# Optimization experiments

Hardware: AMD Instinct MI355X
Metric: run time of the kernel (lower is better)

Reference implementation:

```python
import jax, jax.numpy as jnp
import numpy as np

M = 8192   # output rows
N = 8192   # input dim
K = 8192   # non_zero_rows (inner dim after dropping empty B rows)
NNZ_A = 256  # nonzeros per row of A (m x k)
NNZ_B = 256  # nonzeros per row of B (k x n)
BATCH = 32


def setup_inputs() -> dict:
    key = jax.random.key(0)
    k1, k2, k3, k4, k5 = jax.random.split(key, 5)
    x = jax.random.normal(k1, (N, BATCH), dtype=jnp.float32)
    a_idx = jax.random.randint(k2, (M, NNZ_A), 0, K, dtype=jnp.int32)
    a_vals = jax.random.normal(k3, (M, NNZ_A), dtype=jnp.float32) * 0.05
    b_idx = jax.random.randint(k4, (K, NNZ_B), 0, N, dtype=jnp.int32)
    b_vals = jax.random.normal(k5, (K, NNZ_B), dtype=jnp.float32) * 0.05
    return {"x": x, "a_idx": a_idx, "a_vals": a_vals, "b_idx": b_idx, "b_vals": b_vals}


def reference(x, a_idx, a_vals, b_idx, b_vals):
    # Double-sparse matvec: y = A @ (B @ x), sparse matrices in ELL form
    # (row-wise column indices + values, equivalent math to the CSR kernel).
    # B @ x: gather x rows per nonzero of B, contract over nnz axis.
    bx = jnp.einsum('kj,kjb->kb', b_vals, x[b_idx])        # [K, BATCH]
    # A @ bx: gather bx rows per nonzero of A.
    y = jnp.einsum('mj,mjb->mb', a_vals, bx[a_idx])        # [M, BATCH]
    # Match torch output layout: (1, batch, m)
    return y.T[None]
```

## Files before the change

kernel.cpp:

```cpp
#include <hip/hip_runtime.h>


#define NNZ     256
#define BATCH   32
#define ROWS    8192
#define SEGR    2048
#define NSEG    4
#define RPB     32
#define THREADS 512

typedef int      vi4 __attribute__((ext_vector_type(4)));
typedef float    vf4 __attribute__((ext_vector_type(4)));
typedef _Float16 vh2 __attribute__((ext_vector_type(2)));
typedef _Float16 vh4 __attribute__((ext_vector_type(4)));
typedef _Float16 vh8 __attribute__((ext_vector_type(8)));

union V8 { vh8 h8; vh2 h2[4]; unsigned u[4]; };

__global__ __launch_bounds__(256) void cvt_f32_f16(
    const float* __restrict__ src, _Float16* __restrict__ dst)
{
    const int i = blockIdx.x * 256 + threadIdx.x;
    const vf4 v = *(const vf4*)(src + i * 4);
    vh4 h;
    h.x = (_Float16)v.x; h.y = (_Float16)v.y;
    h.z = (_Float16)v.z; h.w = (_Float16)v.w;
    *(vh4*)(dst + i * 4) = h;
}

static __device__ __forceinline__ unsigned hpack(float f)
{
    const unsigned short u = __builtin_bit_cast(unsigned short, (_Float16)f);
    return ((unsigned)u << 16) | (unsigned)u;
}

#define PROC(K, BB)                                                           \
    do {                                                                      \
        const int k_ = (K);                                                   \
        V8 xv_;                                                               \
        xv_.h8 = *(const vh8*)(lb + ((((unsigned)k_ & 2047u) << 6) + soffb)); \
        const unsigned sel_ = ((k_ >> 11) == p) ? (BB) : 0u;                  \
        const vh2 b2_ = __builtin_bit_cast(vh2, sel_);                        \
        acc[t].h2[0] += b2_ * xv_.h2[0];                                      \
        acc[t].h2[1] += b2_ * xv_.h2[1];                                      \
        acc[t].h2[2] += b2_ * xv_.h2[2];                                      \
        acc[t].h2[3] += b2_ * xv_.h2[3];                                      \
    } while (0)

template <bool OUT16>
__global__ __launch_bounds__(THREADS, 2) void ell_spmv_lds(
    const int*      __restrict__ idx,
    const float*    __restrict__ vals,
    const _Float16* __restrict__ src,
    _Float16*       __restrict__ dst16,
    float*          __restrict__ dst32)
{
    __shared__ __attribute__((aligned(16))) _Float16 lds[SEGR * BATCH];

    const int tid   = threadIdx.x;
    const int wave  = tid >> 6;
    const int lane  = tid & 63;
    const int s     = lane & 3;
    const int q     = lane >> 2;
    const int soffb = s * 16;
    const int rbase = blockIdx.x * RPB;

    vi4      iv[4][4];
    unsigned hh[4][16];
    #pragma unroll
    for (int t = 0; t < 4; ++t) {
        const int r = rbase + wave * 4 + t;
        const vi4* i4 = (const vi4*)(idx  + (size_t)r * NNZ) + q * 4;
        const vf4* v4 = (const vf4*)(vals + (size_t)r * NNZ) + q * 4;
        vf4 vv[4];
        #pragma unroll
        for (int u = 0; u < 4; ++u) iv[t][u] = __builtin_nontemporal_load(i4 + u);
        #pragma unroll
        for (int u = 0; u < 4; ++u) vv[u]    = __builtin_nontemporal_load(v4 + u);
        #pragma unroll
        for (int u = 0; u < 4; ++u) {
            hh[t][4*u+0] = hpack(vv[u].x);
            hh[t][4*u+1] = hpack(vv[u].y);
            hh[t][4*u+2] = hpack(vv[u].z);
            hh[t][4*u+3] = hpack(vv[u].w);
        }
    }

    V8 acc[4];
    #pragma unroll
    for (int t = 0; t < 4; ++t) {
        acc[t].u[0] = 0; acc[t].u[1] = 0; acc[t].u[2] = 0; acc[t].u[3] = 0;
    }

    const char* lb = (const char*)lds;

    #pragma unroll 1
    for (int p = 0; p < NSEG; ++p) {
        __syncthreads();
        const char* gseg = (const char*)(src + (size_t)p * SEGR * BATCH);
        #pragma unroll
        for (int tch = 0; tch < 16; ++tch) {
            const int off = tch * 8192 + tid * 16;
            __builtin_amdgcn_global_load_lds(
                (const __attribute__((address_space(1))) unsigned int*)(gseg + off),
                (__attribute__((address_space(3))) unsigned int*)((char*)lds + off),
                16, 0, 0);
        }
        __syncthreads();

        #pragma unroll
        for (int t = 0; t < 4; ++t) {
            #pragma unroll
            for (int u = 0; u < 4; ++u) {
                PROC(iv[t][u].x, hh[t][4*u+0]);
                PROC(iv[t][u].y, hh[t][4*u+1]);
                PROC(iv[t][u].z, hh[t][4*u+2]);
                PROC(iv[t][u].w, hh[t][4*u+3]);
            }
        }
    }

    float* tile = (float*)lds;
    if (!OUT16) __syncthreads();

    #pragma unroll
    for (int t = 0; t < 4; ++t) {
        float a32[8];
        #pragma unroll
        for (int j = 0; j < 8; ++j) a32[j] = (float)acc[t].h8[j];
        #pragma unroll
        for (int d = 4; d < 64; d <<= 1) {
            #pragma unroll
            for (int j = 0; j < 8; ++j) a32[j] += __shfl_xor(a32[j], d);
        }
        if (OUT16) {
            if (q == 0) {
                const int r = rbase + wave * 4 + t;
                vh8 h;
                #pragma unroll
                for (int j = 0; j < 8; ++j) h[j] = (_Float16)a32[j];
                *(vh8*)(dst16 + (size_t)r * BATCH + s * 8) = h;
            }
        } else {
            if (q == 0) {
                const int rl = wave * 4 + t;
                #pragma unroll
                for (int j = 0; j < 8; ++j) tile[rl * 33 + s * 8 + j] = a32[j];
            }
        }
    }

    if (!OUT16) {
        __syncthreads();
        const int e  = tid * 2;
        const int b  = e >> 5;
        const int rr = e & 31;
        float2 v2;
        v2.x = tile[rr * 33 + b];
        v2.y = tile[(rr + 1) * 33 + b];
        *(float2*)(dst32 + (size_t)b * ROWS + rbase + rr) = v2;
    }
}

#undef PROC

extern "C" void kernel_launch(void* const* d_in, const int* in_sizes, int n_in,
                              void* d_out, int out_size, void* d_ws, size_t ws_size,
                              hipStream_t stream) {
    (void)in_sizes; (void)n_in; (void)out_size; (void)ws_size;
    const float* x      = (const float*)d_in[0];
    const int*   a_idx  = (const int*)  d_in[1];
    const float* a_vals = (const float*)d_in[2];
    const int*   b_idx  = (const int*)  d_in[3];
    const float* b_vals = (const float*)d_in[4];
    float*       out    = (float*)d_out;

    _Float16* bx16 = (_Float16*)d_ws;
    _Float16* x16  = (_Float16*)d_ws + (size_t)ROWS * BATCH;

    cvt_f32_f16<<<dim3(ROWS * BATCH / 4 / 256), dim3(256), 0, stream>>>(x, x16);
    ell_spmv_lds<true ><<<dim3(ROWS / RPB), dim3(THREADS), 0, stream>>>(
        b_idx, b_vals, x16, bx16, nullptr);
    ell_spmv_lds<false><<<dim3(ROWS / RPB), dim3(THREADS), 0, stream>>>(
        a_idx, a_vals, bx16, nullptr, out);
}
```

Measured before the change: 127.1 us.

## Fuse conversion and both SpMV passes into one persistent kernel with grid barriers

Replaces the three launches (f32-to-f16 convert, B pass, A pass) with one kernel that synchronises all 256 blocks through global atomic barriers. It also prefetches A's indices and values into registers before the second barrier so that load overlaps the barrier wait. Masked-out gathers now read a fixed LDS address instead of the real index. The aim is to remove launch gaps and tail effects between stages. The barrier only works if every block is co-resident, which holds with 256 blocks at two per CU on this part, and holding two row-register sets raises register pressure.

```diff
diff --git a/kernel.cpp b/kernel.cpp
--- a/kernel.cpp
+++ b/kernel.cpp
@@ -8,25 +8,16 @@
 #define NSEG    4
 #define RPB     32
 #define THREADS 512
+#define BLOCKS  (ROWS / RPB)
 
 typedef int      vi4 __attribute__((ext_vector_type(4)));
 typedef float    vf4 __attribute__((ext_vector_type(4)));
 typedef _Float16 vh2 __attribute__((ext_vector_type(2)));
-typedef _Float16 vh4 __attribute__((ext_vector_type(4)));
 typedef _Float16 vh8 __attribute__((ext_vector_type(8)));
 
 union V8 { vh8 h8; vh2 h2[4]; unsigned u[4]; };
 
-__global__ __launch_bounds__(256) void cvt_f32_f16(
-    const float* __restrict__ src, _Float16* __restrict__ dst)
-{
-    const int i = blockIdx.x * 256 + threadIdx.x;
-    const vf4 v = *(const vf4*)(src + i * 4);
-    vh4 h;
-    h.x = (_Float16)v.x; h.y = (_Float16)v.y;
-    h.z = (_Float16)v.z; h.w = (_Float16)v.w;
-    *(vh4*)(dst + i * 4) = h;
-}
+struct RowRegs { vi4 iv[4][4]; unsigned hh[4][16]; };
 
 static __device__ __forceinline__ unsigned hpack(float f)
 {
@@ -34,26 +25,107 @@
     return ((unsigned)u << 16) | (unsigned)u;
 }
 
-#define PROC(K, BB)                                                           \
-    do {                                                                      \
-        const int k_ = (K);                                                   \
-        V8 xv_;                                                               \
-        xv_.h8 = *(const vh8*)(lb + ((((unsigned)k_ & 2047u) << 6) + soffb)); \
-        const unsigned sel_ = ((k_ >> 11) == p) ? (BB) : 0u;                  \
-        const vh2 b2_ = __builtin_bit_cast(vh2, sel_);                        \
-        acc[t].h2[0] += b2_ * xv_.h2[0];                                      \
-        acc[t].h2[1] += b2_ * xv_.h2[1];                                      \
-        acc[t].h2[2] += b2_ * xv_.h2[2];                                      \
-        acc[t].h2[3] += b2_ * xv_.h2[3];                                      \
-    } while (0)
-
-template <bool OUT16>
-__global__ __launch_bounds__(THREADS, 2) void ell_spmv_lds(
-    const int*      __restrict__ idx,
-    const float*    __restrict__ vals,
-    const _Float16* __restrict__ src,
-    _Float16*       __restrict__ dst16,
-    float*          __restrict__ dst32)
+static __device__ __forceinline__ void load_rows(
+    const int* __restrict__ idx, const float* __restrict__ vals,
+    int r0, int q, RowRegs& R)
+{
+    #pragma unroll
+    for (int t = 0; t < 4; ++t) {
+        const vi4* i4 = (const vi4*)(idx  + (size_t)(r0 + t) * NNZ) + q * 4;
+        const vf4* v4 = (const vf4*)(vals + (size_t)(r0 + t) * NNZ) + q * 4;
+        vf4 vv[4];
+        #pragma unroll
+        for (int u = 0; u < 4; ++u) R.iv[t][u] = __builtin_nontemporal_load(i4 + u);
+        #pragma unroll
+        for (int u = 0; u < 4; ++u) vv[u]      = __builtin_nontemporal_load(v4 + u);
+        #pragma unroll
+        for (int u = 0; u < 4; ++u) {
+            R.hh[t][4*u+0] = hpack(vv[u].x);
+            R.hh[t][4*u+1] = hpack(vv[u].y);
+            R.hh[t][4*u+2] = hpack(vv[u].z);
+            R.hh[t][4*u+3] = hpack(vv[u].w);
+        }
+    }
+}
+
+static __device__ __forceinline__ void proc1(
+    int k, unsigned bb, int p, const char* lb, int soffb, V8& a)
+{
+    const bool in = (((unsigned)k >> 11) == (unsigned)p);
+    const int  ra = ((k & 2047) << 6) + soffb;
+    const int  ad = in ? ra : soffb;
+    V8 xv;
+    xv.h8 = *(const vh8*)(lb + ad);
+    const vh2 b2 = __builtin_bit_cast(vh2, in ? bb : 0u);
+    a.h2[0] += b2 * xv.h2[0];
+    a.h2[1] += b2 * xv.h2[1];
+    a.h2[2] += b2 * xv.h2[2];
+    a.h2[3] += b2 * xv.h2[3];
+}
+
+static __device__ __forceinline__ void pass4(
+    const RowRegs& R, const _Float16* __restrict__ src,
+    _Float16* lds, int tid, int soffb, V8 acc[4])
+{
+    const char* lb = (const char*)lds;
+    #pragma unroll 1
+    for (int p = 0; p < NSEG; ++p) {
+        __syncthreads();
+        const char* gseg = (const char*)(src + (size_t)p * SEGR * BATCH);
+        #pragma unroll
+        for (int tch = 0; tch < 16; ++tch) {
+            const int off = tch * 8192 + tid * 16;
+            __builtin_amdgcn_global_load_lds(
+                (const __attribute__((address_space(1))) unsigned int*)(gseg + off),
+                (__attribute__((address_space(3))) unsigned int*)((char*)lds + off),
+                16, 0, 0);
+        }
+        __syncthreads();
+
+        #pragma unroll
+        for (int t = 0; t < 4; ++t) {
+            #pragma unroll
+            for (int u = 0; u < 4; ++u) {
+                proc1(R.iv[t][u].x, R.hh[t][4*u+0], p, lb, soffb, acc[t]);
+                proc1(R.iv[t][u].y, R.hh[t][4*u+1], p, lb, soffb, acc[t]);
+                proc1(R.iv[t][u].z, R.hh[t][4*u+2], p, lb, soffb, acc[t]);
+                proc1(R.iv[t][u].w, R.hh[t][4*u+3], p, lb, soffb, acc[t]);
+            }
+        }
+    }
+}
+
+static __device__ __forceinline__ void gridbar(unsigned* bar, unsigned target)
+{
+    __syncthreads();
+    if (threadIdx.x == 0) {
+        __threadfence();
+        __hip_atomic_fetch_add(bar, 1u, __ATOMIC_ACQ_REL, __HIP_MEMORY_SCOPE_AGENT);
+        while (__hip_atomic_load(bar, __ATOMIC_ACQUIRE, __HIP_MEMORY_SCOPE_AGENT)
+               < target) {
+            __builtin_amdgcn_s_sleep(8);
+        }
+        __threadfence();
+    }
+    __syncthreads();
+}
+
+__global__ void bar_init(unsigned* bar)
+{
+    if (threadIdx.x == 0)
+        __hip_atomic_store(bar, 0u, __ATOMIC_RELEASE, __HIP_MEMORY_SCOPE_AGENT);
+}
+
+__global__ __launch_bounds__(THREADS, 2) void fused_spmv(
+    const float* __restrict__ x,
+    const int*   __restrict__ a_idx,
+    const float* __restrict__ a_vals,
+    const int*   __restrict__ b_idx,
+    const float* __restrict__ b_vals,
+    _Float16*    __restrict__ x16,
+    _Float16*    __restrict__ bx16,
+    float*       __restrict__ out,
+    unsigned*    __restrict__ bar)
 {
     __shared__ __attribute__((aligned(16))) _Float16 lds[SEGR * BATCH];
 
@@ -64,65 +136,55 @@
     const int q     = lane >> 2;
     const int soffb = s * 16;
     const int rbase = blockIdx.x * RPB;
-
-    vi4      iv[4][4];
-    unsigned hh[4][16];
-    #pragma unroll
-    for (int t = 0; t < 4; ++t) {
-        const int r = rbase + wave * 4 + t;
-        const vi4* i4 = (const vi4*)(idx  + (size_t)r * NNZ) + q * 4;
-        const vf4* v4 = (const vf4*)(vals + (size_t)r * NNZ) + q * 4;
-        vf4 vv[4];
-        #pragma unroll
-        for (int u = 0; u < 4; ++u) iv[t][u] = __builtin_nontemporal_load(i4 + u);
-        #pragma unroll
-        for (int u = 0; u < 4; ++u) vv[u]    = __builtin_nontemporal_load(v4 + u);
-        #pragma unroll
-        for (int u = 0; u < 4; ++u) {
-            hh[t][4*u+0] = hpack(vv[u].x);
-            hh[t][4*u+1] = hpack(vv[u].y);
-            hh[t][4*u+2] = hpack(vv[u].z);
-            hh[t][4*u+3] = hpack(vv[u].w);
-        }
-    }
+    const int r0    = rbase + wave * 4;
+
+    RowRegs RB;
+    load_rows(b_idx, b_vals, r0, q, RB);
+    {
+        const int gid = blockIdx.x * THREADS + tid;
+        const float2 v = ((const float2*)x)[gid];
+        vh2 h; h.x = (_Float16)v.x; h.y = (_Float16)v.y;
+        ((vh2*)x16)[gid] = h;
+    }
+    gridbar(bar, BLOCKS);
 
     V8 acc[4];
     #pragma unroll
     for (int t = 0; t < 4; ++t) {
         acc[t].u[0] = 0; acc[t].u[1] = 0; acc[t].u[2] = 0; acc[t].u[3] = 0;
     }
-
-    const char* lb = (const char*)lds;
-
-    #pragma unroll 1
-    for (int p = 0; p < NSEG; ++p) {
-        __syncthreads();
-        const char* gseg = (const char*)(src + (size_t)p * SEGR * BATCH);
-        #pragma unroll
-        for (int tch = 0; tch < 16; ++tch) {
-            const int off = tch * 8192 + tid * 16;
-            __builtin_amdgcn_global_load_lds(
-                (const __attribute__((address_space(1))) unsigned int*)(gseg + off),
-                (__attribute__((address_space(3))) unsigned int*)((char*)lds + off),
-                16, 0, 0);
-        }
-        __syncthreads();
-
-        #pragma unroll
-        for (int t = 0; t < 4; ++t) {
-            #pragma unroll
-            for (int u = 0; u < 4; ++u) {
-                PROC(iv[t][u].x, hh[t][4*u+0]);
-                PROC(iv[t][u].y, hh[t][4*u+1]);
-                PROC(iv[t][u].z, hh[t][4*u+2]);
-                PROC(iv[t][u].w, hh[t][4*u+3]);
-            }
-        }
-    }
-
+    pass4(RB, x16, lds, tid, soffb, acc);
+
+    RowRegs RA;
+    load_rows(a_idx, a_vals, r0, q, RA);
+
+    #pragma unroll
+    for (int t = 0; t < 4; ++t) {
+        float a32[8];
+        #pragma unroll
+        for (int j = 0; j < 8; ++j) a32[j] = (float)acc[t].h8[j];
+        #pragma unroll
+        for (int d = 4; d < 64; d <<= 1) {
+            #pragma unroll
+            for (int j = 0; j < 8; ++j) a32[j] += __shfl_xor(a32[j], d);
+        }
+        if (q == 0) {
+            vh8 h;
+            #pragma unroll
+            for (int j = 0; j < 8; ++j) h[j] = (_Float16)a32[j];
+            *(vh8*)(bx16 + (size_t)(r0 + t) * BATCH + s * 8) = h;
+        }
+    }
+    gridbar(bar, 2 * BLOCKS);
+
+    #pragma unroll
+    for (int t = 0; t < 4; ++t) {
+        acc[t].u[0] = 0; acc[t].u[1] = 0; acc[t].u[2] = 0; acc[t].u[3] = 0;
+    }
+    pass4(RA, bx16, lds, tid, soffb, acc);
+
+    __syncthreads();
     float* tile = (float*)lds;
-    if (!OUT16) __syncthreads();
-
     #pragma unroll
     for (int t = 0; t < 4; ++t) {
         float a32[8];
@@ -133,36 +195,23 @@
             #pragma unroll
             for (int j = 0; j < 8; ++j) a32[j] += __shfl_xor(a32[j], d);
         }
-        if (OUT16) {
-            if (q == 0) {
-                const int r = rbase + wave * 4 + t;
-                vh8 h;
-                #pragma unroll
-                for (int j = 0; j < 8; ++j) h[j] = (_Float16)a32[j];
-                *(vh8*)(dst16 + (size_t)r * BATCH + s * 8) = h;
-            }
-        } else {
-            if (q == 0) {
-                const int rl = wave * 4 + t;
-                #pragma unroll
-                for (int j = 0; j < 8; ++j) tile[rl * 33 + s * 8 + j] = a32[j];
-            }
-        }
-    }
-
-    if (!OUT16) {
-        __syncthreads();
+        if (q == 0) {
+            const int rl = wave * 4 + t;
+            #pragma unroll
+            for (int j = 0; j < 8; ++j) tile[rl * 33 + s * 8 + j] = a32[j];
+        }
+    }
+    __syncthreads();
+    {
         const int e  = tid * 2;
         const int b  = e >> 5;
         const int rr = e & 31;
         float2 v2;
         v2.x = tile[rr * 33 + b];
         v2.y = tile[(rr + 1) * 33 + b];
-        *(float2*)(dst32 + (size_t)b * ROWS + rbase + rr) = v2;
-    }
-}
-
-#undef PROC
+        *(float2*)(out + (size_t)b * ROWS + rbase + rr) = v2;
+    }
+}
 
 extern "C" void kernel_launch(void* const* d_in, const int* in_sizes, int n_in,
                               void* d_out, int out_size, void* d_ws, size_t ws_size,
@@ -176,11 +225,11 @@
     float*       out    = (float*)d_out;
 
     _Float16* bx16 = (_Float16*)d_ws;
-    _Float16* x16  = (_Float16*)d_ws + (size_t)ROWS * BATCH;
-
-    cvt_f32_f16<<<dim3(ROWS * BATCH / 4 / 256), dim3(256), 0, stream>>>(x, x16);
-    ell_spmv_lds<true ><<<dim3(ROWS / RPB), dim3(THREADS), 0, stream>>>(
-        b_idx, b_vals, x16, bx16, nullptr);
-    ell_spmv_lds<false><<<dim3(ROWS / RPB), dim3(THREADS), 0, stream>>>(
-        a_idx, a_vals, bx16, nullptr, out);
-}
+    _Float16* x16  = bx16 + (size_t)ROWS * BATCH;
+    unsigned* bar  = (unsigned*)((char*)d_ws +
+                                 (size_t)2 * ROWS * BATCH * sizeof(_Float16));
+
+    bar_init<<<dim3(1), dim3(64), 0, stream>>>(bar);
+    fused_spmv<<<dim3(BLOCKS), dim3(THREADS), 0, stream>>>(
+        x, a_idx, a_vals, b_idx, b_vals, x16, bx16, out, bar);
+}
```

Measured after the change: 184.8 us. 1.45x slower.

## Pre-bin sparse entries by segment into packed half/index words

Applied to the files above, without the earlier changes.

Adds a preprocessing kernel that converts x to fp16 and, for both A and B, reorders each row's nonzeros by which 2048-row segment of the dense operand they hit. Each entry is packed as an fp16 value plus a 16-bit index, and per-segment offsets are stored. The SpMV kernels then process only the entries for the current segment instead of masking all 256 per segment, which removes the 4x redundant gather/FMA work. The packed entries are staged in LDS, and the next segment's table load is issued early. In exchange, a pre-pass over both index arrays is added each call, LDS use rises because the entries buffer is added, and the inner loop's trip count now varies per row.

```diff
diff --git a/kernel.cpp b/kernel.cpp
--- a/kernel.cpp
+++ b/kernel.cpp
@@ -8,54 +8,108 @@
 #define NSEG    4
 #define RPB     32
 #define THREADS 512
+#define BLOCKS  (ROWS / RPB)
 
 typedef int      vi4 __attribute__((ext_vector_type(4)));
 typedef float    vf4 __attribute__((ext_vector_type(4)));
 typedef _Float16 vh2 __attribute__((ext_vector_type(2)));
-typedef _Float16 vh4 __attribute__((ext_vector_type(4)));
 typedef _Float16 vh8 __attribute__((ext_vector_type(8)));
 
 union V8 { vh8 h8; vh2 h2[4]; unsigned u[4]; };
 
-__global__ __launch_bounds__(256) void cvt_f32_f16(
-    const float* __restrict__ src, _Float16* __restrict__ dst)
+static __device__ __forceinline__ void gll16(const char* g, char* l)
 {
-    const int i = blockIdx.x * 256 + threadIdx.x;
-    const vf4 v = *(const vf4*)(src + i * 4);
-    vh4 h;
-    h.x = (_Float16)v.x; h.y = (_Float16)v.y;
-    h.z = (_Float16)v.z; h.w = (_Float16)v.w;
-    *(vh4*)(dst + i * 4) = h;
-}
-
-static __device__ __forceinline__ unsigned hpack(float f)
+    __builtin_amdgcn_global_load_lds(
+        (const __attribute__((address_space(1))) unsigned int*)g,
+        (__attribute__((address_space(3))) unsigned int*)l, 16, 0, 0);
+}
+
+__global__ __launch_bounds__(256) void bin_cvt(
+    const float* __restrict__ x,
+    const int*   __restrict__ a_idx, const float* __restrict__ a_vals,
+    const int*   __restrict__ b_idx, const float* __restrict__ b_vals,
+    _Float16* __restrict__ x16,
+    unsigned* __restrict__ bentB, unsigned long long* __restrict__ offB,
+    unsigned* __restrict__ bentA, unsigned long long* __restrict__ offA)
 {
-    const unsigned short u = __builtin_bit_cast(unsigned short, (_Float16)f);
-    return ((unsigned)u << 16) | (unsigned)u;
-}
-
-#define PROC(K, BB)                                                           \
-    do {                                                                      \
-        const int k_ = (K);                                                   \
-        V8 xv_;                                                               \
-        xv_.h8 = *(const vh8*)(lb + ((((unsigned)k_ & 2047u) << 6) + soffb)); \
-        const unsigned sel_ = ((k_ >> 11) == p) ? (BB) : 0u;                  \
-        const vh2 b2_ = __builtin_bit_cast(vh2, sel_);                        \
-        acc[t].h2[0] += b2_ * xv_.h2[0];                                      \
-        acc[t].h2[1] += b2_ * xv_.h2[1];                                      \
-        acc[t].h2[2] += b2_ * xv_.h2[2];                                      \
-        acc[t].h2[3] += b2_ * xv_.h2[3];                                      \
-    } while (0)
+    __shared__ __attribute__((aligned(16))) unsigned sent[4][NNZ];
+
+    const int tid  = threadIdx.x;
+    const int wave = tid >> 6;
+    const int lane = tid & 63;
+
+    {
+        const int gid = blockIdx.x * 256 + tid;
+        x16[gid] = (_Float16)x[gid];
+    }
+
+    const unsigned long long lt = (1ull << lane) - 1ull;
+    const int wgid = blockIdx.x * 4 + wave;
+
+    #pragma unroll
+    for (int w = 0; w < 4; ++w) {
+        const bool isB = (w < 2);
+        const int  r   = wgid + (w & 1) * 4096;
+        const int*   idx  = isB ? b_idx  : a_idx;
+        const float* vals = isB ? b_vals : a_vals;
+        unsigned*           bent = isB ? bentB : bentA;
+        unsigned long long* off  = isB ? offB  : offA;
+
+        const vi4 kk = __builtin_nontemporal_load(
+            (const vi4*)(idx + (size_t)r * NNZ) + lane);
+        const vf4 vv = __builtin_nontemporal_load(
+            (const vf4*)(vals + (size_t)r * NNZ) + lane);
+
+        unsigned c0 = 0, c1 = 0, c2 = 0, c3 = 0;
+        int sg[4]; unsigned rk[4];
+        #pragma unroll
+        for (int j = 0; j < 4; ++j) {
+            const int sgn = kk[j] >> 11;
+            const unsigned long long m0 = __ballot(sgn == 0);
+            const unsigned long long m1 = __ballot(sgn == 1);
+            const unsigned long long m2 = __ballot(sgn == 2);
+            const unsigned long long m3 = __ballot(sgn == 3);
+            rk[j] = (sgn == 0) ? c0 + (unsigned)__popcll(m0 & lt)
+                  : (sgn == 1) ? c1 + (unsigned)__popcll(m1 & lt)
+                  : (sgn == 2) ? c2 + (unsigned)__popcll(m2 & lt)
+                  :              c3 + (unsigned)__popcll(m3 & lt);
+            sg[j] = sgn;
+            c0 += (unsigned)__popcll(m0); c1 += (unsigned)__popcll(m1);
+            c2 += (unsigned)__popcll(m2); c3 += (unsigned)__popcll(m3);
+        }
+        const unsigned b1 = c0, b2 = c0 + c1, b3 = c0 + c1 + c2;
+
+        #pragma unroll
+        for (int j = 0; j < 4; ++j) {
+            const unsigned base = (sg[j] == 0) ? 0u : (sg[j] == 1) ? b1
+                                 : (sg[j] == 2) ? b2 : b3;
+            const unsigned short hv =
+                __builtin_bit_cast(unsigned short, (_Float16)vv[j]);
+            sent[wave][base + rk[j]] =
+                ((unsigned)hv << 16) | ((unsigned)kk[j] & 0xFFFFu);
+        }
+        __syncthreads();
+
+        const vi4 ob = *(const vi4*)&sent[wave][lane * 4];
+        *(vi4*)(bent + (size_t)r * NNZ + lane * 4) = ob;
+        if (lane == 0)
+            off[r] = ((unsigned long long)b1 << 16) |
+                     ((unsigned long long)b2 << 32) |
+                     ((unsigned long long)b3 << 48);
+        __syncthreads();
+    }
+}
 
 template <bool OUT16>
-__global__ __launch_bounds__(THREADS, 2) void ell_spmv_lds(
-    const int*      __restrict__ idx,
-    const float*    __restrict__ vals,
+__global__ __launch_bounds__(THREADS) void ell_spmv_bin(
+    const unsigned* __restrict__ bent,
+    const unsigned long long* __restrict__ off,
     const _Float16* __restrict__ src,
-    _Float16*       __restrict__ dst16,
-    float*          __restrict__ dst32)
+    _Float16* __restrict__ dst16,
+    float*    __restrict__ dst32)
 {
-    __shared__ __attribute__((aligned(16))) _Float16 lds[SEGR * BATCH];
+    __shared__ __attribute__((aligned(16))) _Float16 table[SEGR * BATCH];
+    __shared__ __attribute__((aligned(16))) unsigned entl[RPB * NNZ];
 
     const int tid   = threadIdx.x;
     const int wave  = tid >> 6;
@@ -64,64 +118,67 @@
     const int q     = lane >> 2;
     const int soffb = s * 16;
     const int rbase = blockIdx.x * RPB;
-
-    vi4      iv[4][4];
-    unsigned hh[4][16];
+    const int r0    = rbase + wave * 4;
+
+    {
+        const char* ge = (const char*)(bent + (size_t)rbase * NNZ);
+        #pragma unroll
+        for (int u = 0; u < 4; ++u)
+            gll16(ge + u * 8192 + tid * 16, (char*)entl + u * 8192 + tid * 16);
+        const char* gs = (const char*)src;
+        #pragma unroll
+        for (int u = 0; u < 16; ++u)
+            gll16(gs + u * 8192 + tid * 16, (char*)table + u * 8192 + tid * 16);
+    }
+
+    int nof[4][5];
     #pragma unroll
     for (int t = 0; t < 4; ++t) {
-        const int r = rbase + wave * 4 + t;
-        const vi4* i4 = (const vi4*)(idx  + (size_t)r * NNZ) + q * 4;
-        const vf4* v4 = (const vf4*)(vals + (size_t)r * NNZ) + q * 4;
-        vf4 vv[4];
-        #pragma unroll
-        for (int u = 0; u < 4; ++u) iv[t][u] = __builtin_nontemporal_load(i4 + u);
-        #pragma unroll
-        for (int u = 0; u < 4; ++u) vv[u]    = __builtin_nontemporal_load(v4 + u);
-        #pragma unroll
-        for (int u = 0; u < 4; ++u) {
-            hh[t][4*u+0] = hpack(vv[u].x);
-            hh[t][4*u+1] = hpack(vv[u].y);
-            hh[t][4*u+2] = hpack(vv[u].z);
-            hh[t][4*u+3] = hpack(vv[u].w);
-        }
+        const unsigned long long o = off[r0 + t];
+        nof[t][0] = (int)(o & 0xFFFFull);
+        nof[t][1] = (int)((o >> 16) & 0xFFFFull);
+        nof[t][2] = (int)((o >> 32) & 0xFFFFull);
+        nof[t][3] = (int)((o >> 48) & 0xFFFFull);
+        nof[t][4] = NNZ;
     }
 
     V8 acc[4];
     #pragma unroll
     for (int t = 0; t < 4; ++t) {
-        acc[t].u[0] = 0; acc[t].u[1] = 0; acc[t].u[2] = 0; acc[t].u[3] = 0;
-    }
-
-    const char* lb = (const char*)lds;
-
-    #pragma unroll 1
+        acc[t].u[0] = acc[t].u[1] = acc[t].u[2] = acc[t].u[3] = 0;
+    }
+
+    __syncthreads();
+
+    #pragma unroll
     for (int p = 0; p < NSEG; ++p) {
-        __syncthreads();
-        const char* gseg = (const char*)(src + (size_t)p * SEGR * BATCH);
-        #pragma unroll
-        for (int tch = 0; tch < 16; ++tch) {
-            const int off = tch * 8192 + tid * 16;
-            __builtin_amdgcn_global_load_lds(
-                (const __attribute__((address_space(1))) unsigned int*)(gseg + off),
-                (__attribute__((address_space(3))) unsigned int*)((char*)lds + off),
-                16, 0, 0);
-        }
-        __syncthreads();
-
         #pragma unroll
         for (int t = 0; t < 4; ++t) {
+            const int n1 = nof[t][p + 1];
+            #pragma unroll 2
+            for (int i = nof[t][p] + q; i < n1; i += 16) {
+                const unsigned e  = entl[(wave * 4 + t) * NNZ + i];
+                const unsigned bb = (e & 0xFFFF0000u) | (e >> 16);
+                V8 xv;
+                xv.h8 = *(const vh8*)((const char*)table +
+                                      ((e & 2047u) << 6) + soffb);
+                const vh2 b2 = __builtin_bit_cast(vh2, bb);
+                acc[t].h2[0] += b2 * xv.h2[0];
+                acc[t].h2[1] += b2 * xv.h2[1];
+                acc[t].h2[2] += b2 * xv.h2[2];
+                acc[t].h2[3] += b2 * xv.h2[3];
+            }
+        }
+        if (p < NSEG - 1) {
+            __syncthreads();
+            const char* gs = (const char*)src + (size_t)(p + 1) * (SEGR * 64);
             #pragma unroll
-            for (int u = 0; u < 4; ++u) {
-                PROC(iv[t][u].x, hh[t][4*u+0]);
-                PROC(iv[t][u].y, hh[t][4*u+1]);
-                PROC(iv[t][u].z, hh[t][4*u+2]);
-                PROC(iv[t][u].w, hh[t][4*u+3]);
-            }
-        }
-    }
-
-    float* tile = (float*)lds;
-    if (!OUT16) __syncthreads();
+            for (int u = 0; u < 16; ++u)
+                gll16(gs + u * 8192 + tid * 16,
+                      (char*)table + u * 8192 + tid * 16);
+            __syncthreads();
+        }
+    }
 
     #pragma unroll
     for (int t = 0; t < 4; ++t) {
@@ -135,13 +192,14 @@
         }
         if (OUT16) {
             if (q == 0) {
-                const int r = rbase + wave * 4 + t;
                 vh8 h;
                 #pragma unroll
                 for (int j = 0; j < 8; ++j) h[j] = (_Float16)a32[j];
-                *(vh8*)(dst16 + (size_t)r * BATCH + s * 8) = h;
+                *(vh8*)(dst16 + (size_t)(r0 + t) * BATCH + s * 8) = h;
             }
         } else {
+            if (t == 0) __syncthreads();
+            float* tile = (float*)table;
             if (q == 0) {
                 const int rl = wave * 4 + t;
                 #pragma unroll
@@ -152,6 +210,7 @@
 
     if (!OUT16) {
         __syncthreads();
+        float* tile = (float*)table;
         const int e  = tid * 2;
         const int b  = e >> 5;
         const int rr = e & 31;
@@ -161,8 +220,6 @@
         *(float2*)(dst32 + (size_t)b * ROWS + rbase + rr) = v2;
     }
 }
-
-#undef PROC
 
 extern "C" void kernel_launch(void* const* d_in, const int* in_sizes, int n_in,
                               void* d_out, int out_size, void* d_ws, size_t ws_size,
@@ -175,12 +232,20 @@
     const float* b_vals = (const float*)d_in[4];
     float*       out    = (float*)d_out;
 
-    _Float16* bx16 = (_Float16*)d_ws;
-    _Float16* x16  = (_Float16*)d_ws + (size_t)ROWS * BATCH;
-
-    cvt_f32_f16<<<dim3(ROWS * BATCH / 4 / 256), dim3(256), 0, stream>>>(x, x16);
-    ell_spmv_lds<true ><<<dim3(ROWS / RPB), dim3(THREADS), 0, stream>>>(
-        b_idx, b_vals, x16, bx16, nullptr);
-    ell_spmv_lds<false><<<dim3(ROWS / RPB), dim3(THREADS), 0, stream>>>(
-        a_idx, a_vals, bx16, nullptr, out);
-}
+    char* w = (char*)d_ws;
+    _Float16* x16   = (_Float16*)(w);
+    _Float16* bx16  = (_Float16*)(w + (1u << 19));
+    unsigned* bentB = (unsigned*)(w + (1u << 20));
+    unsigned* bentA = (unsigned*)(w + 9 * (1u << 20));
+    unsigned long long* offB =
+        (unsigned long long*)(w + 17 * (1u << 20));
+    unsigned long long* offA =
+        (unsigned long long*)(w + 17 * (1u << 20) + (1u << 16));
+
+    bin_cvt<<<dim3(1024), dim3(256), 0, stream>>>(
+        x, a_idx, a_vals, b_idx, b_vals, x16, bentB, offB, bentA, offA);
+    ell_spmv_bin<true ><<<dim3(BLOCKS), dim3(THREADS), 0, stream>>>(
+        bentB, offB, x16, bx16, nullptr);
+    ell_spmv_bin<false><<<dim3(BLOCKS), dim3(THREADS), 0, stream>>>(
+        bentA, offA, bx16, nullptr, out);
+}
```

Measured after the change: 121.9 us. -4.1%, faster.
